# Optimization experiments

Measured on AMD Instinct MI355X. Metric: run time of the kernel, lower is better.

## Reference

```python
import jax, jax.numpy as jnp
import numpy as np

EMBED = 1024
HEADS = 16
HEAD_DIM = EMBED // HEADS
HIDDEN = 4 * EMBED
EPS = 1e-5


def layer_norm(x, g, b):
    mu = jnp.mean(x, axis=-1, keepdims=True)
    var = jnp.var(x, axis=-1, keepdims=True)
    return (x - mu) * jax.lax.rsqrt(var + EPS) * g + b


def setup_inputs() -> dict:
    key = jax.random.key(0)
    ks = jax.random.split(key, 12)
    s_e = 1.0 / np.sqrt(EMBED)
    s_h = 1.0 / np.sqrt(HIDDEN)
    return {
        "x": jax.random.normal(ks[0], (8, 1024, EMBED), dtype=jnp.float32),
        "ln1_g": jnp.ones((EMBED,), jnp.float32),
        "ln1_b": jnp.zeros((EMBED,), jnp.float32),
        "w_qkv": jax.random.normal(ks[1], (EMBED, 3 * EMBED), jnp.float32) * s_e,
        "b_qkv": jax.random.normal(ks[2], (3 * EMBED,), jnp.float32) * s_e,
        "w_out": jax.random.normal(ks[3], (EMBED, EMBED), jnp.float32) * s_e,
        "b_out": jax.random.normal(ks[4], (EMBED,), jnp.float32) * s_e,
        "ln2_g": jnp.ones((EMBED,), jnp.float32),
        "ln2_b": jnp.zeros((EMBED,), jnp.float32),
        "w_up": jax.random.normal(ks[5], (EMBED, HIDDEN), jnp.float32) * s_e,
        "b_up": jax.random.normal(ks[6], (HIDDEN,), jnp.float32) * s_e,
        "w_down": jax.random.normal(ks[7], (HIDDEN, EMBED), jnp.float32) * s_h,
        "b_down": jax.random.normal(ks[8], (EMBED,), jnp.float32) * s_h,
    }


def reference(x, ln1_g, ln1_b, w_qkv, b_qkv, w_out, b_out,
              ln2_g, ln2_b, w_up, b_up, w_down, b_down):
    B, T, C = x.shape
    # --- attention sub-block ---
    h = layer_norm(x, ln1_g, ln1_b)
    qkv = h @ w_qkv + b_qkv                                   # [B,T,3C]
    q, k, v = jnp.split(qkv, 3, axis=-1)
    def heads(t):  # [B,T,C] -> [B,H,T,D]
        return t.reshape(B, T, HEADS, HEAD_DIM).transpose(0, 2, 1, 3)
    q, k, v = heads(q), heads(k), heads(v)
    scale = HEAD_DIM ** -0.5
    attn = jax.nn.softmax(jnp.einsum('bhqd,bhkd->bhqk', q, k) * scale, axis=-1)
    y = jnp.einsum('bhqk,bhkd->bhqd', attn, v)                # [B,H,T,D]
    y = y.transpose(0, 2, 1, 3).reshape(B, T, C)
    x = x + y @ w_out + b_out
    # --- MLP sub-block ---
    h = layer_norm(x, ln2_g, ln2_b)
    h = jax.nn.relu(h @ w_up + b_up)
    x = x + h @ w_down + b_down
    return x
```

## Files before the change

kernel.cpp:

```cpp
#include <hip/hip_runtime.h>
#include <stdint.h>


typedef __attribute__((ext_vector_type(8))) short short8;
typedef __attribute__((ext_vector_type(4))) short short4v;
typedef __attribute__((ext_vector_type(4))) float floatx4;

#define NROWS 8192

__device__ __forceinline__ unsigned short f2bf(float f) {
    union { float f; unsigned u; } x; x.f = f;
    unsigned r = x.u + 0x7fffu + ((x.u >> 16) & 1u);
    return (unsigned short)(r >> 16);
}
__device__ __forceinline__ float bf2f(unsigned short h) {
    union { unsigned u; float f; } x; x.u = (unsigned)h << 16; return x.f;
}

__device__ __forceinline__ void gl2lds16(const unsigned short* g, unsigned short* l) {
    __builtin_amdgcn_global_load_lds(
        (const __attribute__((address_space(1))) unsigned int*)(uintptr_t)g,
        (__attribute__((address_space(3))) unsigned int*)(unsigned int)(uintptr_t)l,
        16, 0, 0);
}

__global__ __launch_bounds__(256) void prep_kernel(
    const float* __restrict__ w_qkv, const float* __restrict__ w_out,
    const float* __restrict__ w_up, const float* __restrict__ w_down,
    unsigned short* __restrict__ wqkvT, unsigned short* __restrict__ woutT,
    unsigned short* __restrict__ wupT, unsigned short* __restrict__ wdownT,
    const float* __restrict__ x, const float* __restrict__ g,
    const float* __restrict__ b, unsigned short* __restrict__ h1)
{
    int bid = blockIdx.x;
    __shared__ unsigned short tile[32][33];
    __shared__ float rs[4], rs2[4];
    if (bid < 12288) {
        const float* in; unsigned short* out; int K, N, nb, tb;
        if (bid < 3072)      { in = w_qkv;  out = wqkvT;  K = 1024; N = 3072; nb = 96;  tb = bid; }
        else if (bid < 4096) { in = w_out;  out = woutT;  K = 1024; N = 1024; nb = 32;  tb = bid - 3072; }
        else if (bid < 8192) { in = w_up;   out = wupT;   K = 1024; N = 4096; nb = 128; tb = bid - 4096; }
        else                 { in = w_down; out = wdownT; K = 4096; N = 1024; nb = 32;  tb = bid - 8192; }
        int n0 = (tb % nb) * 32, k0 = (tb / nb) * 32;
        int tx = threadIdx.x & 31, ty = threadIdx.x >> 5;
        #pragma unroll
        for (int i = 0; i < 4; ++i)
            tile[ty + i * 8][tx] = f2bf(in[(size_t)(k0 + ty + i * 8) * N + n0 + tx]);
        __syncthreads();
        #pragma unroll
        for (int i = 0; i < 4; ++i)
            out[(size_t)(n0 + ty + i * 8) * K + k0 + tx] = tile[tx][ty + i * 8];
    } else {
        int row = bid - 12288, t = threadIdx.x;
        const float4* xr = (const float4*)(x + (size_t)row * 1024);
        float4 v = xr[t];
        float s  = v.x + v.y + v.z + v.w;
        float s2 = v.x * v.x + v.y * v.y + v.z * v.z + v.w * v.w;
        #pragma unroll
        for (int off = 32; off; off >>= 1) {
            s  += __shfl_xor(s,  off, 64);
            s2 += __shfl_xor(s2, off, 64);
        }
        int w = t >> 6;
        if ((t & 63) == 0) { rs[w] = s; rs2[w] = s2; }
        __syncthreads();
        s  = rs[0] + rs[1] + rs[2] + rs[3];
        s2 = rs2[0] + rs2[1] + rs2[2] + rs2[3];
        float mean = s * (1.0f / 1024.0f);
        float var  = s2 * (1.0f / 1024.0f) - mean * mean;
        float rstd = rsqrtf(var + 1e-5f);
        float4 gv = ((const float4*)g)[t];
        float4 bv = ((const float4*)b)[t];
        ushort4 o;
        o.x = f2bf((v.x - mean) * rstd * gv.x + bv.x);
        o.y = f2bf((v.y - mean) * rstd * gv.y + bv.y);
        o.z = f2bf((v.z - mean) * rstd * gv.z + bv.z);
        o.w = f2bf((v.w - mean) * rstd * gv.w + bv.w);
        ((ushort4*)(h1 + (size_t)row * 1024))[t] = o;
    }
}

__global__ __launch_bounds__(256) void ln_bf16b(
    const unsigned short* __restrict__ x, const float* __restrict__ g,
    const float* __restrict__ b, unsigned short* __restrict__ out)
{
    int row = blockIdx.x, t = threadIdx.x;
    ushort4 hv = ((const ushort4*)(x + (size_t)row * 1024))[t];
    float v0 = bf2f(hv.x), v1 = bf2f(hv.y), v2 = bf2f(hv.z), v3 = bf2f(hv.w);
    float s  = v0 + v1 + v2 + v3;
    float s2 = v0 * v0 + v1 * v1 + v2 * v2 + v3 * v3;
    #pragma unroll
    for (int off = 32; off; off >>= 1) {
        s  += __shfl_xor(s,  off, 64);
        s2 += __shfl_xor(s2, off, 64);
    }
    __shared__ float rs[4], rs2[4];
    int w = t >> 6;
    if ((t & 63) == 0) { rs[w] = s; rs2[w] = s2; }
    __syncthreads();
    s  = rs[0] + rs[1] + rs[2] + rs[3];
    s2 = rs2[0] + rs2[1] + rs2[2] + rs2[3];
    float mean = s * (1.0f / 1024.0f);
    float var  = s2 * (1.0f / 1024.0f) - mean * mean;
    float rstd = rsqrtf(var + 1e-5f);
    float4 gv = ((const float4*)g)[t];
    float4 bv = ((const float4*)b)[t];
    ushort4 o;
    o.x = f2bf((v0 - mean) * rstd * gv.x + bv.x);
    o.y = f2bf((v1 - mean) * rstd * gv.y + bv.y);
    o.z = f2bf((v2 - mean) * rstd * gv.z + bv.z);
    o.w = f2bf((v3 - mean) * rstd * gv.w + bv.w);
    ((ushort4*)(out + (size_t)row * 1024))[t] = o;
}

template <int MODE>
__global__ __launch_bounds__(256, 2) void gemm_dbuf(
    const unsigned short* __restrict__ A, const unsigned short* __restrict__ Bt,
    int M, int N, int K,
    const float* __restrict__ bias,
    const float* __restrict__ residF, const unsigned short* __restrict__ residB,
    float* __restrict__ outF, unsigned short* __restrict__ outB)
{
    int m0 = blockIdx.x * 128, n0 = blockIdx.y * 128;
    int tid = threadIdx.x;
    int w = tid >> 6, l = tid & 63, quad = l >> 4, lr = l & 15;
    int wm = w & 1, wn = w >> 1;

    __shared__ unsigned short As[2][128 * 64];
    __shared__ unsigned short Bs[2][128 * 64];

    floatx4 acc[4][4];
    #pragma unroll
    for (int i = 0; i < 4; ++i)
        #pragma unroll
        for (int j = 0; j < 4; ++j)
            acc[i][j] = (floatx4){0.f, 0.f, 0.f, 0.f};

    int srow = l >> 3;
    int scol = ((l & 7) ^ srow) * 8;
    const unsigned short* Ag = A  + (size_t)(m0 + 32 * w + srow) * K + scol;
    const unsigned short* Bg = Bt + (size_t)(n0 + 32 * w + srow) * K + scol;

    #pragma unroll
    for (int u = 0; u < 4; ++u) {
        gl2lds16(Ag + (size_t)(8 * u) * K, &As[0][(32 * w + 8 * u) * 64]);
        gl2lds16(Bg + (size_t)(8 * u) * K, &Bs[0][(32 * w + 8 * u) * 64]);
    }
    __syncthreads();

    for (int kt = 0; kt < K; kt += 64) {
        int cur = (kt >> 6) & 1;
        if (kt + 64 < K) {
            #pragma unroll
            for (int u = 0; u < 4; ++u) {
                gl2lds16(Ag + (size_t)(8 * u) * K + kt + 64,
                         &As[cur ^ 1][(32 * w + 8 * u) * 64]);
                gl2lds16(Bg + (size_t)(8 * u) * K + kt + 64,
                         &Bs[cur ^ 1][(32 * w + 8 * u) * 64]);
            }
        }
        short8 af[4][2], bf[4][2];
        #pragma unroll
        for (int i = 0; i < 4; ++i)
            #pragma unroll
            for (int s = 0; s < 2; ++s)
                af[i][s] = *(const short8*)
                    &As[cur][(64 * wm + 16 * i + lr) * 64 + (((s * 4 + quad) ^ (lr & 7)) * 8)];
        #pragma unroll
        for (int j = 0; j < 4; ++j)
            #pragma unroll
            for (int s = 0; s < 2; ++s)
                bf[j][s] = *(const short8*)
                    &Bs[cur][(64 * wn + 16 * j + lr) * 64 + (((s * 4 + quad) ^ (lr & 7)) * 8)];
        #pragma unroll
        for (int i = 0; i < 4; ++i)
            #pragma unroll
            for (int j = 0; j < 4; ++j) {
                acc[i][j] = __builtin_amdgcn_mfma_f32_16x16x32_bf16(
                    af[i][0], bf[j][0], acc[i][j], 0, 0, 0);
                acc[i][j] = __builtin_amdgcn_mfma_f32_16x16x32_bf16(
                    af[i][1], bf[j][1], acc[i][j], 0, 0, 0);
            }
        __syncthreads();
    }

    #pragma unroll
    for (int i = 0; i < 4; ++i)
        #pragma unroll
        for (int j = 0; j < 4; ++j)
            #pragma unroll
            for (int r = 0; r < 4; ++r) {
                int m = m0 + 64 * wm + 16 * i + quad * 4 + r;
                int n = n0 + 64 * wn + 16 * j + lr;
                float c = acc[i][j][r] + bias[n];
                if (MODE == 1)
                    outB[(size_t)m * N + n] = f2bf(c + residF[(size_t)m * N + n]);
                else
                    outF[(size_t)m * N + n] = c + bf2f(residB[(size_t)m * N + n]);
            }
}

template <int MODE>
__global__ __launch_bounds__(256, 2) void gemm_mfma(
    const unsigned short* __restrict__ A, const unsigned short* __restrict__ Bt,
    int M, int N, int K,
    const float* __restrict__ bias,
    unsigned short* __restrict__ outB,
    unsigned short* __restrict__ qO, unsigned short* __restrict__ kO,
    unsigned short* __restrict__ vO)
{
    constexpr int TN = 256, NJ = 8, TNH = 128;
    int m0 = blockIdx.x * 128, n0 = blockIdx.y * TN;
    int tid = threadIdx.x;
    int w = tid >> 6, l = tid & 63, quad = l >> 4, lr = l & 15;
    int wm = w & 1, wn = w >> 1;

    __shared__ unsigned short As[128 * 32];
    __shared__ unsigned short Bs[TN * 32];

    floatx4 acc[4][NJ];
    #pragma unroll
    for (int i = 0; i < 4; ++i)
        #pragma unroll
        for (int j = 0; j < NJ; ++j)
            acc[i][j] = (floatx4){0.f, 0.f, 0.f, 0.f};

    int srow = l >> 2;
    int scol = (l & 3) * 8;
    const unsigned short* Ag = A  + (size_t)(m0 + w * 32 + srow) * K + scol;
    const unsigned short* Bg = Bt + (size_t)(n0 + w * 64 + srow) * K + scol;
    unsigned short* As0 = &As[(w * 32) * 32];
    unsigned short* As1 = &As[(w * 32 + 16) * 32];
    unsigned short* Bsw = &Bs[(w * 64) * 32];

    for (int kt = 0; kt < K; kt += 32) {
        gl2lds16(Ag + kt, As0);
        gl2lds16(Ag + (size_t)16 * K + kt, As1);
        #pragma unroll
        for (int u = 0; u < 4; ++u)
            gl2lds16(Bg + (size_t)(16 * u) * K + kt, Bsw + (16 * u) * 32);
        __syncthreads();
        short8 af[4], bf[NJ];
        #pragma unroll
        for (int i = 0; i < 4; ++i)
            af[i] = *(const short8*)&As[(64 * wm + 16 * i + lr) * 32 + quad * 8];
        #pragma unroll
        for (int j = 0; j < NJ; ++j)
            bf[j] = *(const short8*)&Bs[(TNH * wn + 16 * j + lr) * 32 + quad * 8];
        #pragma unroll
        for (int i = 0; i < 4; ++i)
            #pragma unroll
            for (int j = 0; j < NJ; ++j)
                acc[i][j] = __builtin_amdgcn_mfma_f32_16x16x32_bf16(
                    af[i], bf[j], acc[i][j], 0, 0, 0);
        __syncthreads();
    }

    if (MODE == 0) {
        int sel = n0 >> 10;
        if (sel < 2) {
            const float qscale = (sel == 0) ? 0.125f : 1.0f;
            unsigned short* dst = (sel == 0) ? qO : kO;
            #pragma unroll
            for (int i = 0; i < 4; ++i)
                #pragma unroll
                for (int j = 0; j < NJ; ++j)
                    #pragma unroll
                    for (int r = 0; r < 4; ++r) {
                        int m = m0 + 64 * wm + 16 * i + quad * 4 + r;
                        int n = n0 + TNH * wn + 16 * j + lr;
                        float c = (acc[i][j][r] + bias[n]) * qscale;
                        int bb = m >> 10, t = m & 1023;
                        int cc = n & 1023, h = cc >> 6, d = cc & 63;
                        dst[(((size_t)(bb * 16 + h)) * 1024 + t) * 64 + d] = f2bf(c);
                    }
        } else {
            int bb = m0 >> 10;
            #pragma unroll
            for (int i = 0; i < 4; ++i) {
                int t0 = (m0 & 1023) + 64 * wm + 16 * i + quad * 4;
                #pragma unroll
                for (int j = 0; j < NJ; ++j) {
                    int n = n0 + TNH * wn + 16 * j + lr;
                    int cc = n & 1023, h = cc >> 6, d = cc & 63;
                    float bn = bias[n];
                    ushort4 pk;
                    pk.x = f2bf(acc[i][j][0] + bn);
                    pk.y = f2bf(acc[i][j][1] + bn);
                    pk.z = f2bf(acc[i][j][2] + bn);
                    pk.w = f2bf(acc[i][j][3] + bn);
                    *(ushort4*)&vO[((size_t)(bb * 16 + h) * 64 + d) * 1024 + t0] = pk;
                }
            }
        }
    } else {
        #pragma unroll
        for (int i = 0; i < 4; ++i)
            #pragma unroll
            for (int j = 0; j < NJ; ++j)
                #pragma unroll
                for (int r = 0; r < 4; ++r) {
                    int m = m0 + 64 * wm + 16 * i + quad * 4 + r;
                    int n = n0 + TNH * wn + 16 * j + lr;
                    outB[(size_t)m * N + n] = f2bf(fmaxf(acc[i][j][r] + bias[n], 0.f));
                }
    }
}

__global__ __launch_bounds__(256, 2) void attn_kernel(
    const unsigned short* __restrict__ qg, const unsigned short* __restrict__ kg,
    const unsigned short* __restrict__ vtg, unsigned short* __restrict__ y)
{
    int bid = blockIdx.x;
    int bh = bid & 127, qt = bid >> 7;
    int b = bh >> 4, h = bh & 15;
    int tid = threadIdx.x;
    int w = tid >> 6, l = tid & 63, quad = l >> 4, lr = l & 15;

    __shared__ unsigned short Qs[128 * 64];
    __shared__ unsigned short Ks[2][64 * 64];
    __shared__ unsigned short Vs[2][64 * 64];
    __shared__ unsigned short Ps[4][32 * 68];

    int srow = l >> 3;
    int scol = ((l & 7) ^ srow) * 8;

    {
        const unsigned short* qbase = qg + (size_t)bh * 65536 + (size_t)(qt * 128) * 64;
        #pragma unroll
        for (int u = 0; u < 4; ++u)
            gl2lds16(qbase + (size_t)(32 * w + 8 * u + srow) * 64 + scol,
                     &Qs[(32 * w + 8 * u) * 64]);
    }
    const unsigned short* kbase = kg  + (size_t)bh * 65536;
    const unsigned short* vbase = vtg + (size_t)bh * 65536;

    #pragma unroll
    for (int u = 0; u < 2; ++u) {
        gl2lds16(kbase + (size_t)(16 * w + 8 * u + srow) * 64 + scol,
                 &Ks[0][(16 * w + 8 * u) * 64]);
        gl2lds16(vbase + (size_t)(16 * w + 8 * u + srow) * 1024 + scol,
                 &Vs[0][(16 * w + 8 * u) * 64]);
    }
    __syncthreads();

    short8 af[2][2];
    #pragma unroll
    for (int i = 0; i < 2; ++i)
        #pragma unroll
        for (int s = 0; s < 2; ++s)
            af[i][s] = *(const short8*)
                &Qs[(32 * w + 16 * i + lr) * 64 + ((s * 4 + quad) ^ (lr & 7)) * 8];

    floatx4 o[2][4];
    float lsum[2][4];
    #pragma unroll
    for (int i = 0; i < 2; ++i)
        #pragma unroll
        for (int j = 0; j < 4; ++j) o[i][j] = (floatx4){0.f, 0.f, 0.f, 0.f};
    #pragma unroll
    for (int i = 0; i < 2; ++i)
        #pragma unroll
        for (int r = 0; r < 4; ++r) lsum[i][r] = 0.f;

    for (int kt = 0; kt < 16; ++kt) {
        int cur = kt & 1;
        if (kt + 1 < 16) {
            const unsigned short* kb = kbase + (size_t)((kt + 1) * 64) * 64;
            const unsigned short* vb = vbase + (size_t)((kt + 1) * 64);
            #pragma unroll
            for (int u = 0; u < 2; ++u) {
                gl2lds16(kb + (size_t)(16 * w + 8 * u + srow) * 64 + scol,
                         &Ks[cur ^ 1][(16 * w + 8 * u) * 64]);
                gl2lds16(vb + (size_t)(16 * w + 8 * u + srow) * 1024 + scol,
                         &Vs[cur ^ 1][(16 * w + 8 * u) * 64]);
            }
        }

        short8 kf[4][2];
        #pragma unroll
        for (int j = 0; j < 4; ++j)
            #pragma unroll
            for (int s = 0; s < 2; ++s)
                kf[j][s] = *(const short8*)
                    &Ks[cur][(16 * j + lr) * 64 + ((s * 4 + quad) ^ (lr & 7)) * 8];

        floatx4 s[2][4];
        #pragma unroll
        for (int i = 0; i < 2; ++i)
            #pragma unroll
            for (int j = 0; j < 4; ++j) {
                s[i][j] = (floatx4){0.f, 0.f, 0.f, 0.f};
                #pragma unroll
                for (int st = 0; st < 2; ++st)
                    s[i][j] = __builtin_amdgcn_mfma_f32_16x16x32_bf16(
                        af[i][st], kf[j][st], s[i][j], 0, 0, 0);
            }

        #pragma unroll
        for (int i = 0; i < 2; ++i)
            #pragma unroll
            for (int j = 0; j < 4; ++j)
                #pragma unroll
                for (int r = 0; r < 4; ++r) {
                    float p = __expf(s[i][j][r]);
                    lsum[i][r] += p;
                    Ps[w][(16 * i + quad * 4 + r) * 68 + 16 * j + lr] = f2bf(p);
                }

        asm volatile("s_waitcnt lgkmcnt(0)" ::: "memory");

        short8 vf[4][2];
        #pragma unroll
        for (int j = 0; j < 4; ++j)
            #pragma unroll
            for (int s = 0; s < 2; ++s)
                vf[j][s] = *(const short8*)
                    &Vs[cur][(16 * j + lr) * 64 + ((s * 4 + quad) ^ (lr & 7)) * 8];

        #pragma unroll
        for (int i = 0; i < 2; ++i)
            #pragma unroll
            for (int st = 0; st < 2; ++st) {
                short4v p0 = *(const short4v*)&Ps[w][(16 * i + lr) * 68 + st * 32 + quad * 8];
                short4v p1 = *(const short4v*)&Ps[w][(16 * i + lr) * 68 + st * 32 + quad * 8 + 4];
                short8 pf;
                #pragma unroll
                for (int e = 0; e < 4; ++e) { pf[e] = p0[e]; pf[e + 4] = p1[e]; }
                #pragma unroll
                for (int j = 0; j < 4; ++j)
                    o[i][j] = __builtin_amdgcn_mfma_f32_16x16x32_bf16(
                        pf, vf[j][st], o[i][j], 0, 0, 0);
            }
        __syncthreads();
    }

    #pragma unroll
    for (int off = 8; off; off >>= 1)
        #pragma unroll
        for (int i = 0; i < 2; ++i)
            #pragma unroll
            for (int r = 0; r < 4; ++r)
                lsum[i][r] += __shfl_xor(lsum[i][r], off, 64);
    float rinv[2][4];
    #pragma unroll
    for (int i = 0; i < 2; ++i)
        #pragma unroll
        for (int r = 0; r < 4; ++r) rinv[i][r] = 1.0f / lsum[i][r];

    #pragma unroll
    for (int i = 0; i < 2; ++i)
        #pragma unroll
        for (int j = 0; j < 4; ++j)
            #pragma unroll
            for (int r = 0; r < 4; ++r) {
                int trow = qt * 128 + 32 * w + 16 * i + quad * 4 + r;
                int col  = h * 64 + 16 * j + lr;
                y[((size_t)b * 1024 + trow) * 1024 + col] =
                    f2bf(o[i][j][r] * rinv[i][r]);
            }
}

extern "C" void kernel_launch(void* const* d_in, const int* in_sizes, int n_in,
                              void* d_out, int out_size, void* d_ws, size_t ws_size,
                              hipStream_t stream)
{
    const float* x      = (const float*)d_in[0];
    const float* ln1_g  = (const float*)d_in[1];
    const float* ln1_b  = (const float*)d_in[2];
    const float* w_qkv  = (const float*)d_in[3];
    const float* b_qkv  = (const float*)d_in[4];
    const float* w_out  = (const float*)d_in[5];
    const float* b_out  = (const float*)d_in[6];
    const float* ln2_g  = (const float*)d_in[7];
    const float* ln2_b  = (const float*)d_in[8];
    const float* w_up   = (const float*)d_in[9];
    const float* b_up   = (const float*)d_in[10];
    const float* w_down = (const float*)d_in[11];
    const float* b_down = (const float*)d_in[12];

    char* ws = (char*)d_ws;
    unsigned short* wqkvT  = (unsigned short*)(ws + 0);
    unsigned short* woutT  = (unsigned short*)(ws + 6291456);
    unsigned short* wupT   = (unsigned short*)(ws + 8388608);
    unsigned short* wdownT = (unsigned short*)(ws + 16777216);
    unsigned short* x2     = (unsigned short*)(ws + 25165824);
    unsigned short* h1     = (unsigned short*)(ws + 58720256);
    unsigned short* qb     = (unsigned short*)(ws + 75497472);
    unsigned short* kb     = (unsigned short*)(ws + 92274688);
    unsigned short* vtb    = (unsigned short*)(ws + 109051904);
    unsigned short* yb     = (unsigned short*)(ws + 125829120);
    unsigned short* a2     = (unsigned short*)(ws + 75497472);
    unsigned short* h2     = h1;

    prep_kernel<<<20480, 256, 0, stream>>>(
        w_qkv, w_out, w_up, w_down, wqkvT, woutT, wupT, wdownT,
        x, ln1_g, ln1_b, h1);

    gemm_mfma<0><<<dim3(NROWS / 128, 3072 / 256), 256, 0, stream>>>(
        h1, wqkvT, NROWS, 3072, 1024, b_qkv, nullptr, qb, kb, vtb);

    attn_kernel<<<1024, 256, 0, stream>>>(qb, kb, vtb, yb);

    gemm_dbuf<1><<<dim3(NROWS / 128, 1024 / 128), 256, 0, stream>>>(
        yb, woutT, NROWS, 1024, 1024, b_out, x, nullptr, nullptr, x2);

    ln_bf16b<<<NROWS, 256, 0, stream>>>(x2, ln2_g, ln2_b, h2);

    gemm_mfma<2><<<dim3(NROWS / 128, 4096 / 256), 256, 0, stream>>>(
        h2, wupT, NROWS, 4096, 1024, b_up, a2, nullptr, nullptr, nullptr);

    gemm_dbuf<3><<<dim3(NROWS / 128, 1024 / 128), 256, 0, stream>>>(
        a2, wdownT, NROWS, 1024, 4096, b_down, nullptr, x2, (float*)d_out, nullptr);
}
```

Before: 477.3 us.

## Replace 128x256 QKV/up GEMM with double-buffered swizzled 128x128 kernel

Swaps the single-buffered 128x256-tile MFMA GEMM used for the QKV and MLP-up projections for a 128x128-tile kernel. The new kernel double-buffers the global-to-LDS loads so the next K slice streams in while the current one is computed, XOR-swizzles LDS columns to reduce bank conflicts, and raises launch bounds to 3 blocks per CU. The smaller tile halves accumulator registers and doubles the grid, which helps occupancy and latency hiding. The cost is lower arithmetic intensity per block, meaning more global reads of A and B per output.

```diff
diff --git a/kernel.cpp b/kernel.cpp
--- a/kernel.cpp
+++ b/kernel.cpp
@@ -114,6 +114,121 @@
 }
 
 template <int MODE>
+__global__ __launch_bounds__(256, 3) void gemm_db128(
+    const unsigned short* __restrict__ A, const unsigned short* __restrict__ Bt,
+    int M, int N, int K,
+    const float* __restrict__ bias,
+    unsigned short* __restrict__ outB,
+    unsigned short* __restrict__ qO, unsigned short* __restrict__ kO,
+    unsigned short* __restrict__ vO)
+{
+    int m0 = blockIdx.x * 128, n0 = blockIdx.y * 128;
+    int tid = threadIdx.x;
+    int w = tid >> 6, l = tid & 63, quad = l >> 4, lr = l & 15;
+    int wm = w & 1, wn = w >> 1;
+
+    __shared__ unsigned short S[2][256 * 32];
+
+    floatx4 acc[4][4];
+    #pragma unroll
+    for (int i = 0; i < 4; ++i)
+        #pragma unroll
+        for (int j = 0; j < 4; ++j)
+            acc[i][j] = (floatx4){0.f, 0.f, 0.f, 0.f};
+
+    int srow = l >> 2;
+    int scol = ((l & 3) ^ (srow & 3)) * 8;
+    const unsigned short* gp[4];
+    int lofs[4];
+    #pragma unroll
+    for (int u = 0; u < 4; ++u) {
+        int rb = 64 * w + 16 * u;
+        if (rb < 128) gp[u] = A  + (size_t)(m0 + rb + srow) * K + scol;
+        else          gp[u] = Bt + (size_t)(n0 + rb - 128 + srow) * K + scol;
+        lofs[u] = rb * 32;
+    }
+
+    #pragma unroll
+    for (int u = 0; u < 4; ++u) gl2lds16(gp[u], &S[0][lofs[u]]);
+    __syncthreads();
+
+    for (int kt = 0; kt < K; kt += 32) {
+        int cur = (kt >> 5) & 1;
+        if (kt + 32 < K) {
+            #pragma unroll
+            for (int u = 0; u < 4; ++u)
+                gl2lds16(gp[u] + kt + 32, &S[cur ^ 1][lofs[u]]);
+        }
+        short8 af[4], bf[4];
+        #pragma unroll
+        for (int i = 0; i < 4; ++i)
+            af[i] = *(const short8*)
+                &S[cur][(64 * wm + 16 * i + lr) * 32 + ((quad ^ (lr & 3)) * 8)];
+        #pragma unroll
+        for (int j = 0; j < 4; ++j)
+            bf[j] = *(const short8*)
+                &S[cur][(128 + 64 * wn + 16 * j + lr) * 32 + ((quad ^ (lr & 3)) * 8)];
+        #pragma unroll
+        for (int i = 0; i < 4; ++i)
+            #pragma unroll
+            for (int j = 0; j < 4; ++j)
+                acc[i][j] = __builtin_amdgcn_mfma_f32_16x16x32_bf16(
+                    af[i], bf[j], acc[i][j], 0, 0, 0);
+        __syncthreads();
+    }
+
+    if (MODE == 0) {
+        int sel = n0 >> 10;
+        if (sel < 2) {
+            const float qscale = (sel == 0) ? 0.125f : 1.0f;
+            unsigned short* dst = (sel == 0) ? qO : kO;
+            #pragma unroll
+            for (int i = 0; i < 4; ++i)
+                #pragma unroll
+                for (int j = 0; j < 4; ++j)
+                    #pragma unroll
+                    for (int r = 0; r < 4; ++r) {
+                        int m = m0 + 64 * wm + 16 * i + quad * 4 + r;
+                        int n = n0 + 64 * wn + 16 * j + lr;
+                        float c = (acc[i][j][r] + bias[n]) * qscale;
+                        int bb = m >> 10, t = m & 1023;
+                        int cc = n & 1023, h = cc >> 6, d = cc & 63;
+                        dst[(((size_t)(bb * 16 + h)) * 1024 + t) * 64 + d] = f2bf(c);
+                    }
+        } else {
+            int bb = m0 >> 10;
+            #pragma unroll
+            for (int i = 0; i < 4; ++i) {
+                int t0 = (m0 & 1023) + 64 * wm + 16 * i + quad * 4;
+                #pragma unroll
+                for (int j = 0; j < 4; ++j) {
+                    int n = n0 + 64 * wn + 16 * j + lr;
+                    int cc = n & 1023, h = cc >> 6, d = cc & 63;
+                    float bn = bias[n];
+                    ushort4 pk;
+                    pk.x = f2bf(acc[i][j][0] + bn);
+                    pk.y = f2bf(acc[i][j][1] + bn);
+                    pk.z = f2bf(acc[i][j][2] + bn);
+                    pk.w = f2bf(acc[i][j][3] + bn);
+                    *(ushort4*)&vO[((size_t)(bb * 16 + h) * 64 + d) * 1024 + t0] = pk;
+                }
+            }
+        }
+    } else {
+        #pragma unroll
+        for (int i = 0; i < 4; ++i)
+            #pragma unroll
+            for (int j = 0; j < 4; ++j)
+                #pragma unroll
+                for (int r = 0; r < 4; ++r) {
+                    int m = m0 + 64 * wm + 16 * i + quad * 4 + r;
+                    int n = n0 + 64 * wn + 16 * j + lr;
+                    outB[(size_t)m * N + n] = f2bf(fmaxf(acc[i][j][r] + bias[n], 0.f));
+                }
+    }
+}
+
+template <int MODE>
 __global__ __launch_bounds__(256, 2) void gemm_dbuf(
     const unsigned short* __restrict__ A, const unsigned short* __restrict__ Bt,
     int M, int N, int K,
@@ -198,113 +313,6 @@
                 else
                     outF[(size_t)m * N + n] = c + bf2f(residB[(size_t)m * N + n]);
             }
-}
-
-template <int MODE>
-__global__ __launch_bounds__(256, 2) void gemm_mfma(
-    const unsigned short* __restrict__ A, const unsigned short* __restrict__ Bt,
-    int M, int N, int K,
-    const float* __restrict__ bias,
-    unsigned short* __restrict__ outB,
-    unsigned short* __restrict__ qO, unsigned short* __restrict__ kO,
-    unsigned short* __restrict__ vO)
-{
-    constexpr int TN = 256, NJ = 8, TNH = 128;
-    int m0 = blockIdx.x * 128, n0 = blockIdx.y * TN;
-    int tid = threadIdx.x;
-    int w = tid >> 6, l = tid & 63, quad = l >> 4, lr = l & 15;
-    int wm = w & 1, wn = w >> 1;
-
-    __shared__ unsigned short As[128 * 32];
-    __shared__ unsigned short Bs[TN * 32];
-
-    floatx4 acc[4][NJ];
-    #pragma unroll
-    for (int i = 0; i < 4; ++i)
-        #pragma unroll
-        for (int j = 0; j < NJ; ++j)
-            acc[i][j] = (floatx4){0.f, 0.f, 0.f, 0.f};
-
-    int srow = l >> 2;
-    int scol = (l & 3) * 8;
-    const unsigned short* Ag = A  + (size_t)(m0 + w * 32 + srow) * K + scol;
-    const unsigned short* Bg = Bt + (size_t)(n0 + w * 64 + srow) * K + scol;
-    unsigned short* As0 = &As[(w * 32) * 32];
-    unsigned short* As1 = &As[(w * 32 + 16) * 32];
-    unsigned short* Bsw = &Bs[(w * 64) * 32];
-
-    for (int kt = 0; kt < K; kt += 32) {
-        gl2lds16(Ag + kt, As0);
-        gl2lds16(Ag + (size_t)16 * K + kt, As1);
-        #pragma unroll
-        for (int u = 0; u < 4; ++u)
-            gl2lds16(Bg + (size_t)(16 * u) * K + kt, Bsw + (16 * u) * 32);
-        __syncthreads();
-        short8 af[4], bf[NJ];
-        #pragma unroll
-        for (int i = 0; i < 4; ++i)
-            af[i] = *(const short8*)&As[(64 * wm + 16 * i + lr) * 32 + quad * 8];
-        #pragma unroll
-        for (int j = 0; j < NJ; ++j)
-            bf[j] = *(const short8*)&Bs[(TNH * wn + 16 * j + lr) * 32 + quad * 8];
-        #pragma unroll
-        for (int i = 0; i < 4; ++i)
-            #pragma unroll
-            for (int j = 0; j < NJ; ++j)
-                acc[i][j] = __builtin_amdgcn_mfma_f32_16x16x32_bf16(
-                    af[i], bf[j], acc[i][j], 0, 0, 0);
-        __syncthreads();
-    }
-
-    if (MODE == 0) {
-        int sel = n0 >> 10;
-        if (sel < 2) {
-            const float qscale = (sel == 0) ? 0.125f : 1.0f;
-            unsigned short* dst = (sel == 0) ? qO : kO;
-            #pragma unroll
-            for (int i = 0; i < 4; ++i)
-                #pragma unroll
-                for (int j = 0; j < NJ; ++j)
-                    #pragma unroll
-                    for (int r = 0; r < 4; ++r) {
-                        int m = m0 + 64 * wm + 16 * i + quad * 4 + r;
-                        int n = n0 + TNH * wn + 16 * j + lr;
-                        float c = (acc[i][j][r] + bias[n]) * qscale;
-                        int bb = m >> 10, t = m & 1023;
-                        int cc = n & 1023, h = cc >> 6, d = cc & 63;
-                        dst[(((size_t)(bb * 16 + h)) * 1024 + t) * 64 + d] = f2bf(c);
-                    }
-        } else {
-            int bb = m0 >> 10;
-            #pragma unroll
-            for (int i = 0; i < 4; ++i) {
-                int t0 = (m0 & 1023) + 64 * wm + 16 * i + quad * 4;
-                #pragma unroll
-                for (int j = 0; j < NJ; ++j) {
-                    int n = n0 + TNH * wn + 16 * j + lr;
-                    int cc = n & 1023, h = cc >> 6, d = cc & 63;
-                    float bn = bias[n];
-                    ushort4 pk;
-                    pk.x = f2bf(acc[i][j][0] + bn);
-                    pk.y = f2bf(acc[i][j][1] + bn);
-                    pk.z = f2bf(acc[i][j][2] + bn);
-                    pk.w = f2bf(acc[i][j][3] + bn);
-                    *(ushort4*)&vO[((size_t)(bb * 16 + h) * 64 + d) * 1024 + t0] = pk;
-                }
-            }
-        }
-    } else {
-        #pragma unroll
-        for (int i = 0; i < 4; ++i)
-            #pragma unroll
-            for (int j = 0; j < NJ; ++j)
-                #pragma unroll
-                for (int r = 0; r < 4; ++r) {
-                    int m = m0 + 64 * wm + 16 * i + quad * 4 + r;
-                    int n = n0 + TNH * wn + 16 * j + lr;
-                    outB[(size_t)m * N + n] = f2bf(fmaxf(acc[i][j][r] + bias[n], 0.f));
-                }
-    }
 }
 
 __global__ __launch_bounds__(256, 2) void attn_kernel(
@@ -497,7 +505,7 @@
         w_qkv, w_out, w_up, w_down, wqkvT, woutT, wupT, wdownT,
         x, ln1_g, ln1_b, h1);
 
-    gemm_mfma<0><<<dim3(NROWS / 128, 3072 / 256), 256, 0, stream>>>(
+    gemm_db128<0><<<dim3(NROWS / 128, 3072 / 128), 256, 0, stream>>>(
         h1, wqkvT, NROWS, 3072, 1024, b_qkv, nullptr, qb, kb, vtb);
 
     attn_kernel<<<1024, 256, 0, stream>>>(qb, kb, vtb, yb);
@@ -507,7 +515,7 @@
 
     ln_bf16b<<<NROWS, 256, 0, stream>>>(x2, ln2_g, ln2_b, h2);
 
-    gemm_mfma<2><<<dim3(NROWS / 128, 4096 / 256), 256, 0, stream>>>(
+    gemm_db128<2><<<dim3(NROWS / 128, 4096 / 128), 256, 0, stream>>>(
         h2, wupT, NROWS, 4096, 1024, b_up, a2, nullptr, nullptr, nullptr);
 
     gemm_dbuf<3><<<dim3(NROWS / 128, 1024 / 128), 256, 0, stream>>>(
```

New measurement: 441.8 us. 1.08x faster.
